# Optimization experiments

Measured on AMD Instinct MI355X. Metric: run time of the kernel, lower is better.

The kernel has to match this reference:

```python
import jax, jax.numpy as jnp
import numpy as np

B, D, H = 131072, 8, 128  # batch, input_size (condition dims), hidden_size
DROPOUT_PROB = 0.1
NAN_FRAC = 0.15


def setup_inputs() -> dict:
    key = jax.random.key(0)
    k1, k2, k3, k4, k5, k6 = jax.random.split(key, 6)
    labels = jax.random.normal(k1, (B, D), dtype=jnp.float32)
    # NaN marks 'missing condition' -> falls back to embedding table row
    nan_mask = jax.random.uniform(k2, (B, D)) < NAN_FRAC
    labels = jnp.where(nan_mask, jnp.nan, labels)
    emb_w = jax.random.normal(k3, (D, H), dtype=jnp.float32) * 0.02  # embedding_drop.weight
    w1 = jax.random.normal(k4, (D, H), dtype=jnp.float32)           # Linear(1,H).weight per dim
    b1 = jax.random.normal(k5, (D, H), dtype=jnp.float32) * 0.02    # Linear(1,H).bias per dim
    w2 = jax.random.normal(k6, (D, H, H), dtype=jnp.float32) * 0.08 # Linear(H,H,bias=False).weight [out,in]
    return {"labels": labels, "emb_w": emb_w, "w1": w1, "b1": b1, "w2": w2,
            "train": 0, "unconditioned": 0}


def reference(labels, emb_w, w1, b1, w2, train, unconditioned):
    # drop mask per (sample, dim): NaN labels, optional random dropout, or everything
    if unconditioned:
        drop = jnp.ones(labels.shape, dtype=bool)
    else:
        drop = jnp.isnan(labels)
        if train:
            rkey = jax.random.fold_in(jax.random.key(0), 1)
            drop = drop | (jax.random.uniform(rkey, labels.shape) < DROPOUT_PROB)
    safe = jnp.where(drop, 0.0, labels)                      # [B,D] NaN-free
    # per-dim MLP, vectorized over dims: Linear(1,H) -> softmax(H) -> Linear(H,H)
    h1 = safe[:, :, None] * w1[None, :, :] + b1[None, :, :]  # [B,D,H]
    s = jax.nn.softmax(h1, axis=-1)                          # softmax over hidden (dim=1 of [N,H])
    mlp = jnp.einsum('bdh,dkh->bdk', s, w2)                  # [B,D,H]
    emb = jnp.where(drop[:, :, None], emb_w[None, :, :], mlp)
    if train:
        nkey = jax.random.fold_in(jax.random.key(0), 2)
        emb = emb + jax.random.normal(nkey, emb.shape, dtype=emb.dtype)
    return emb.sum(axis=1)                                   # [B,H]
```

## Files before the change

### kernel.cpp

```cpp
#include <hip/hip_runtime.h>
#include <hip/hip_bf16.h>

typedef __attribute__((ext_vector_type(4))) float f32x4;
typedef __attribute__((ext_vector_type(4))) int   i32x4;
typedef __attribute__((ext_vector_type(8))) short s16x8;

#define NB 131072
#define ND 8
#define NH 128
#define BROWS 256
#define MT 4

#if __has_builtin(__builtin_amdgcn_exp2f)
#define EXP2F(x) __builtin_amdgcn_exp2f(x)
#define PRESCALE 1.4426950408889634f
#else
#define EXP2F(x) __expf(x)
#define PRESESCALE_FALLBACK
#define PRESCALE 1.0f
#endif

#if __has_builtin(__builtin_amdgcn_rcpf)
#define RCPF(x) __builtin_amdgcn_rcpf(x)
#else
#define RCPF(x) (1.0f / (x))
#endif

__device__ __forceinline__ unsigned short f2bf(float f){
  unsigned u = __float_as_uint(f);
  u += 0x7fffu + ((u >> 16) & 1u);
  return (unsigned short)(u >> 16);
}

__device__ __forceinline__ unsigned pk2(float lo, float hi){
  return __builtin_amdgcn_perm(__float_as_uint(hi), __float_as_uint(lo), 0x07060302u);
}

__global__ __launch_bounds__(256) void cvt_w2_kernel(const float* __restrict__ src,
                                                     uint4* __restrict__ dst){
  int i = blockIdx.x * 256 + threadIdx.x;
  int d = i >> 11, kb = (i >> 7) & 15, n = i & 127;
  const float* s = src + ((d * 128 + n) * 128 + kb * 8);
  float4 v0 = ((const float4*)s)[0];
  float4 v1 = ((const float4*)s)[1];
  uint4 o;
  o.x = (unsigned)f2bf(v0.x) | ((unsigned)f2bf(v0.y) << 16);
  o.y = (unsigned)f2bf(v0.z) | ((unsigned)f2bf(v0.w) << 16);
  o.z = (unsigned)f2bf(v1.x) | ((unsigned)f2bf(v1.y) << 16);
  o.w = (unsigned)f2bf(v1.z) | ((unsigned)f2bf(v1.w) << 16);
  dst[i] = o;
}

__global__ void cvt_emb_kernel(const float* __restrict__ emb_w, uint4* __restrict__ dst){
  int n = threadIdx.x;
  unsigned e0 = f2bf(emb_w[0*NH + n]), e1 = f2bf(emb_w[1*NH + n]);
  unsigned e2 = f2bf(emb_w[2*NH + n]), e3 = f2bf(emb_w[3*NH + n]);
  unsigned e4 = f2bf(emb_w[4*NH + n]), e5 = f2bf(emb_w[5*NH + n]);
  unsigned e6 = f2bf(emb_w[6*NH + n]), e7 = f2bf(emb_w[7*NH + n]);
  uint4 v;
  v.x = e0 | (e1 << 16);  v.y = e2 | (e3 << 16);
  v.z = e4 | (e5 << 16);  v.w = e6 | (e7 << 16);
  dst[n] = v;
}

__global__ __launch_bounds__(256, 2) void cond_embed_kernel(
    const float* __restrict__ labels,
    const float* __restrict__ w1,
    const float* __restrict__ b1,
    const unsigned short* __restrict__ w2b,
    const unsigned short* __restrict__ embT,
    const int* __restrict__ uncond_p,
    float* __restrict__ out)
{
  __shared__ __align__(16) unsigned short lds_w2[2][NH * NH];
  __shared__ __align__(16) float lds_lab[ND * BROWS];
  __shared__ __align__(16) float lds_w1[ND * NH];
  __shared__ __align__(16) float lds_b1[ND * NH];

  const int tid  = threadIdx.x;
  const int wave = tid >> 6;
  const int lane = tid & 63;
  const int quad = lane >> 4;
  const int l16  = lane & 15;
  const int uncond = uncond_p[0];
  const int blockbase = blockIdx.x * BROWS;

  {
    const float4* src = (const float4*)(labels + blockbase * ND);
    #pragma unroll
    for (int c = 0; c < 2; ++c){
      int i = tid + c * 256;
      float4 v = src[i];
      int row = i >> 1, db = (i & 1) * 4;
      lds_lab[(db + 0) * BROWS + row] = v.x;
      lds_lab[(db + 1) * BROWS + row] = v.y;
      lds_lab[(db + 2) * BROWS + row] = v.z;
      lds_lab[(db + 3) * BROWS + row] = v.w;
    }
  }
  {
    float4 a = ((const float4*)w1)[tid];
    float4 b = ((const float4*)b1)[tid];
    ((float4*)lds_w1)[tid] = (float4){a.x * PRESCALE, a.y * PRESCALE, a.z * PRESCALE, a.w * PRESCALE};
    ((float4*)lds_b1)[tid] = (float4){b.x * PRESCALE, b.y * PRESCALE, b.z * PRESCALE, b.w * PRESCALE};
  }

  auto stage = [&](int d, int buf){
    const unsigned short* g = w2b + d * (NH * NH);
    #pragma unroll
    for (int i = 0; i < 8; ++i){
      int idx = tid + i * 256;
      __builtin_amdgcn_global_load_lds(
          (const __attribute__((address_space(1))) void*)(g + idx * 8),
          (__attribute__((address_space(3))) void*)(&lds_w2[buf][idx * 8]),
          16, 0, 0);
    }
  };

  stage(0, 0);
  __syncthreads();

  f32x4 acc[MT][8];
  #pragma unroll
  for (int mt = 0; mt < MT; ++mt)
    #pragma unroll
    for (int nt = 0; nt < 8; ++nt)
      acc[mt][nt] = (f32x4){0.f, 0.f, 0.f, 0.f};

  const s16x8 bones = (s16x8)((short)0x3F80);

  for (int d = 0; d < ND; ++d){
    const int buf = d & 1;
    if (d < ND - 1) stage(d + 1, buf ^ 1);

    float xs[MT];
    #pragma unroll
    for (int mt = 0; mt < MT; ++mt){
      float x = lds_lab[d * BROWS + wave * 64 + mt * 16 + l16];
      bool drop = (uncond != 0) || (x != x);
      xs[mt] = drop ? 0.f : x;
    }

    s16x8 af[MT][4];
    #pragma unroll
    for (int t = 0; t < 4; ++t){
      const float4* w1q = (const float4*)&lds_w1[d * NH + t * 32 + quad * 8];
      const float4* b1q = (const float4*)&lds_b1[d * NH + t * 32 + quad * 8];
      float4 wa = w1q[0], wb = w1q[1];
      float4 ba = b1q[0], bb = b1q[1];
      #pragma unroll
      for (int mt = 0; mt < MT; ++mt){
        float x = xs[mt];
        float e0 = EXP2F(fmaf(x, wa.x, ba.x));
        float e1 = EXP2F(fmaf(x, wa.y, ba.y));
        float e2 = EXP2F(fmaf(x, wa.z, ba.z));
        float e3 = EXP2F(fmaf(x, wa.w, ba.w));
        float e4 = EXP2F(fmaf(x, wb.x, bb.x));
        float e5 = EXP2F(fmaf(x, wb.y, bb.y));
        float e6 = EXP2F(fmaf(x, wb.z, bb.z));
        float e7 = EXP2F(fmaf(x, wb.w, bb.w));
        i32x4 ai;
        ai[0] = (int)pk2(e0, e1);
        ai[1] = (int)pk2(e2, e3);
        ai[2] = (int)pk2(e4, e5);
        ai[3] = (int)pk2(e6, e7);
        af[mt][t] = __builtin_bit_cast(s16x8, ai);
      }
    }

    f32x4 zr[MT];
    #pragma unroll
    for (int mt = 0; mt < MT; ++mt){
      f32x4 z = (f32x4){0.f, 0.f, 0.f, 0.f};
      #pragma unroll
      for (int t = 0; t < 4; ++t)
        z = __builtin_amdgcn_mfma_f32_16x16x32_bf16(af[mt][t], bones, z, 0, 0, 0);
      float4 xc = *(const float4*)&lds_lab[d * BROWS + wave * 64 + mt * 16 + quad * 4];
      zr[mt][0] = ((uncond != 0) || (xc.x != xc.x)) ? 0.f : RCPF(z[0]);
      zr[mt][1] = ((uncond != 0) || (xc.y != xc.y)) ? 0.f : RCPF(z[1]);
      zr[mt][2] = ((uncond != 0) || (xc.z != xc.z)) ? 0.f : RCPF(z[2]);
      zr[mt][3] = ((uncond != 0) || (xc.w != xc.w)) ? 0.f : RCPF(z[3]);
    }

    #pragma unroll
    for (int nt = 0; nt < 8; ++nt){
      f32x4 tm[MT];
      #pragma unroll
      for (int mt = 0; mt < MT; ++mt) tm[mt] = (f32x4){0.f, 0.f, 0.f, 0.f};
      #pragma unroll
      for (int t = 0; t < 4; ++t){
        s16x8 b = *((const s16x8*)&lds_w2[buf][(t * 512 + quad * 128 + nt * 16 + l16) * 8]);
        #pragma unroll
        for (int mt = 0; mt < MT; ++mt)
          tm[mt] = __builtin_amdgcn_mfma_f32_16x16x32_bf16(af[mt][t], b, tm[mt], 0, 0, 0);
      }
      #pragma unroll
      for (int mt = 0; mt < MT; ++mt)
        #pragma unroll
        for (int r = 0; r < 4; ++r)
          acc[mt][nt][r] = fmaf(tm[mt][r], zr[mt][r], acc[mt][nt][r]);
    }

    if (d < ND - 1) __syncthreads();
  }

  s16x8 aex[MT];
  #pragma unroll
  for (int mt = 0; mt < MT; ++mt){
    s16x8 a = (s16x8)((short)0);
    if (quad == 0){
      int row = wave * 64 + mt * 16 + l16;
      #pragma unroll
      for (int j = 0; j < 8; ++j){
        float x = lds_lab[j * BROWS + row];
        bool drop = (uncond != 0) || (x != x);
        a[j] = drop ? (short)0x3F80 : (short)0;
      }
    }
    aex[mt] = a;
  }
  #pragma unroll
  for (int nt = 0; nt < 8; ++nt){
    s16x8 b = (s16x8)((short)0);
    if (quad == 0) b = __builtin_bit_cast(s16x8, ((const i32x4*)embT)[nt * 16 + l16]);
    #pragma unroll
    for (int mt = 0; mt < MT; ++mt)
      acc[mt][nt] = __builtin_amdgcn_mfma_f32_16x16x32_bf16(aex[mt], b, acc[mt][nt], 0, 0, 0);
  }

  #pragma unroll
  for (int mt = 0; mt < MT; ++mt){
    #pragma unroll
    for (int nt = 0; nt < 8; ++nt){
      #pragma unroll
      for (int r = 0; r < 4; ++r){
        int row = blockbase + wave * 64 + mt * 16 + quad * 4 + r;
        out[row * NH + nt * 16 + l16] = acc[mt][nt][r];
      }
    }
  }
}

extern "C" void kernel_launch(void* const* d_in, const int* in_sizes, int n_in,
                              void* d_out, int out_size, void* d_ws, size_t ws_size,
                              hipStream_t stream){
  const float* labels = (const float*)d_in[0];
  const float* emb_w  = (const float*)d_in[1];
  const float* w1     = (const float*)d_in[2];
  const float* b1     = (const float*)d_in[3];
  const float* w2     = (const float*)d_in[4];
  const int*   uncond = (const int*)d_in[6];
  (void)in_sizes; (void)n_in; (void)out_size; (void)ws_size;

  float* out = (float*)d_out;
  unsigned short* w2b  = (unsigned short*)d_ws;
  unsigned short* embT = w2b + ND * NH * NH;

  cvt_w2_kernel<<<64, 256, 0, stream>>>(w2, (uint4*)w2b);
  cvt_emb_kernel<<<1, 128, 0, stream>>>(emb_w, (uint4*)embT);
  cond_embed_kernel<<<NB / BROWS, 256, 0, stream>>>(labels, w1, b1, w2b, embT, uncond, out);
}
```

Before: 160.7 us.

## Halve rows per block, single-buffer W2 in LDS, raise occupancy target

Each block now handles 128 rows with 2 M-tiles per wave instead of 256 rows with 4. The W2 slice sits in a single LDS buffer loaded synchronously at every dim step, where before a double buffer prefetched the next slice. Launch bounds move to 3 blocks per CU, and the smaller accumulator and LDS footprint are meant to allow more resident waves to hide latency. In exchange, W2 loads no longer overlap compute, each dim step gains an extra barrier, and each W2 byte brought into LDS feeds half as many rows.

```diff
diff --git a/kernel.cpp b/kernel.cpp
--- a/kernel.cpp
+++ b/kernel.cpp
@@ -8,15 +8,14 @@
 #define NB 131072
 #define ND 8
 #define NH 128
-#define BROWS 256
-#define MT 4
+#define BROWS 128
+#define MT 2
 
 #if __has_builtin(__builtin_amdgcn_exp2f)
 #define EXP2F(x) __builtin_amdgcn_exp2f(x)
 #define PRESCALE 1.4426950408889634f
 #else
 #define EXP2F(x) __expf(x)
-#define PRESESCALE_FALLBACK
 #define PRESCALE 1.0f
 #endif
 
@@ -63,7 +62,7 @@
   dst[n] = v;
 }
 
-__global__ __launch_bounds__(256, 2) void cond_embed_kernel(
+__global__ __launch_bounds__(256, 3) void cond_embed_kernel(
     const float* __restrict__ labels,
     const float* __restrict__ w1,
     const float* __restrict__ b1,
@@ -72,7 +71,7 @@
     const int* __restrict__ uncond_p,
     float* __restrict__ out)
 {
-  __shared__ __align__(16) unsigned short lds_w2[2][NH * NH];
+  __shared__ __align__(16) unsigned short lds_w2[NH * NH];
   __shared__ __align__(16) float lds_lab[ND * BROWS];
   __shared__ __align__(16) float lds_w1[ND * NH];
   __shared__ __align__(16) float lds_b1[ND * NH];
@@ -86,17 +85,12 @@
   const int blockbase = blockIdx.x * BROWS;
 
   {
-    const float4* src = (const float4*)(labels + blockbase * ND);
-    #pragma unroll
-    for (int c = 0; c < 2; ++c){
-      int i = tid + c * 256;
-      float4 v = src[i];
-      int row = i >> 1, db = (i & 1) * 4;
-      lds_lab[(db + 0) * BROWS + row] = v.x;
-      lds_lab[(db + 1) * BROWS + row] = v.y;
-      lds_lab[(db + 2) * BROWS + row] = v.z;
-      lds_lab[(db + 3) * BROWS + row] = v.w;
-    }
+    float4 v = ((const float4*)(labels + blockbase * ND))[tid];
+    int row = tid >> 1, db = (tid & 1) * 4;
+    lds_lab[(db + 0) * BROWS + row] = v.x;
+    lds_lab[(db + 1) * BROWS + row] = v.y;
+    lds_lab[(db + 2) * BROWS + row] = v.z;
+    lds_lab[(db + 3) * BROWS + row] = v.w;
   }
   {
     float4 a = ((const float4*)w1)[tid];
@@ -105,21 +99,6 @@
     ((float4*)lds_b1)[tid] = (float4){b.x * PRESCALE, b.y * PRESCALE, b.z * PRESCALE, b.w * PRESCALE};
   }
 
-  auto stage = [&](int d, int buf){
-    const unsigned short* g = w2b + d * (NH * NH);
-    #pragma unroll
-    for (int i = 0; i < 8; ++i){
-      int idx = tid + i * 256;
-      __builtin_amdgcn_global_load_lds(
-          (const __attribute__((address_space(1))) void*)(g + idx * 8),
-          (__attribute__((address_space(3))) void*)(&lds_w2[buf][idx * 8]),
-          16, 0, 0);
-    }
-  };
-
-  stage(0, 0);
-  __syncthreads();
-
   f32x4 acc[MT][8];
   #pragma unroll
   for (int mt = 0; mt < MT; ++mt)
@@ -130,13 +109,24 @@
   const s16x8 bones = (s16x8)((short)0x3F80);
 
   for (int d = 0; d < ND; ++d){
-    const int buf = d & 1;
-    if (d < ND - 1) stage(d + 1, buf ^ 1);
+    __syncthreads();
+    {
+      const unsigned short* g = w2b + d * (NH * NH);
+      #pragma unroll
+      for (int i = 0; i < 8; ++i){
+        int idx = tid + i * 256;
+        __builtin_amdgcn_global_load_lds(
+            (const __attribute__((address_space(1))) void*)(g + idx * 8),
+            (__attribute__((address_space(3))) void*)(lds_w2 + idx * 8),
+            16, 0, 0);
+      }
+    }
+    __syncthreads();
 
     float xs[MT];
     #pragma unroll
     for (int mt = 0; mt < MT; ++mt){
-      float x = lds_lab[d * BROWS + wave * 64 + mt * 16 + l16];
+      float x = lds_lab[d * BROWS + wave * 32 + mt * 16 + l16];
       bool drop = (uncond != 0) || (x != x);
       xs[mt] = drop ? 0.f : x;
     }
@@ -175,7 +165,7 @@
       #pragma unroll
       for (int t = 0; t < 4; ++t)
         z = __builtin_amdgcn_mfma_f32_16x16x32_bf16(af[mt][t], bones, z, 0, 0, 0);
-      float4 xc = *(const float4*)&lds_lab[d * BROWS + wave * 64 + mt * 16 + quad * 4];
+      float4 xc = *(const float4*)&lds_lab[d * BROWS + wave * 32 + mt * 16 + quad * 4];
       zr[mt][0] = ((uncond != 0) || (xc.x != xc.x)) ? 0.f : RCPF(z[0]);
       zr[mt][1] = ((uncond != 0) || (xc.y != xc.y)) ? 0.f : RCPF(z[1]);
       zr[mt][2] = ((uncond != 0) || (xc.z != xc.z)) ? 0.f : RCPF(z[2]);
@@ -184,24 +174,20 @@
 
     #pragma unroll
     for (int nt = 0; nt < 8; ++nt){
-      f32x4 tm[MT];
-      #pragma unroll
-      for (int mt = 0; mt < MT; ++mt) tm[mt] = (f32x4){0.f, 0.f, 0.f, 0.f};
+      f32x4 t0 = (f32x4){0.f,0.f,0.f,0.f};
+      f32x4 t1 = (f32x4){0.f,0.f,0.f,0.f};
       #pragma unroll
       for (int t = 0; t < 4; ++t){
-        s16x8 b = *((const s16x8*)&lds_w2[buf][(t * 512 + quad * 128 + nt * 16 + l16) * 8]);
-        #pragma unroll
-        for (int mt = 0; mt < MT; ++mt)
-          tm[mt] = __builtin_amdgcn_mfma_f32_16x16x32_bf16(af[mt][t], b, tm[mt], 0, 0, 0);
-      }
-      #pragma unroll
-      for (int mt = 0; mt < MT; ++mt)
-        #pragma unroll
-        for (int r = 0; r < 4; ++r)
-          acc[mt][nt][r] = fmaf(tm[mt][r], zr[mt][r], acc[mt][nt][r]);
-    }
-
-    if (d < ND - 1) __syncthreads();
+        s16x8 b = *((const s16x8*)&lds_w2[(t * 512 + quad * 128 + nt * 16 + l16) * 8]);
+        t0 = __builtin_amdgcn_mfma_f32_16x16x32_bf16(af[0][t], b, t0, 0, 0, 0);
+        t1 = __builtin_amdgcn_mfma_f32_16x16x32_bf16(af[1][t], b, t1, 0, 0, 0);
+      }
+      #pragma unroll
+      for (int r = 0; r < 4; ++r){
+        acc[0][nt][r] = fmaf(t0[r], zr[0][r], acc[0][nt][r]);
+        acc[1][nt][r] = fmaf(t1[r], zr[1][r], acc[1][nt][r]);
+      }
+    }
   }
 
   s16x8 aex[MT];
@@ -209,7 +195,7 @@
   for (int mt = 0; mt < MT; ++mt){
     s16x8 a = (s16x8)((short)0);
     if (quad == 0){
-      int row = wave * 64 + mt * 16 + l16;
+      int row = wave * 32 + mt * 16 + l16;
       #pragma unroll
       for (int j = 0; j < 8; ++j){
         float x = lds_lab[j * BROWS + row];
@@ -234,7 +220,7 @@
     for (int nt = 0; nt < 8; ++nt){
       #pragma unroll
       for (int r = 0; r < 4; ++r){
-        int row = blockbase + wave * 64 + mt * 16 + quad * 4 + r;
+        int row = blockbase + wave * 32 + mt * 16 + quad * 4 + r;
         out[row * NH + nt * 16 + l16] = acc[mt][nt][r];
       }
     }
```

Result: faster. 136.8 us (-14.9%).
